# Optimization experiments

Hardware: AMD Instinct MI355X
Metric: run time of the kernel (lower is better)

## Reference

```python
import jax, jax.numpy as jnp
import numpy as np

NODE_NUMS = 128
IN_SIZE = 256
OUT_SIZE = 256
BATCH = 4096


def setup_inputs() -> dict:
    key = jax.random.key(0)
    k1, k2, k3, k4, k5 = jax.random.split(key, 5)
    # Xavier-uniform bounds
    limit_w = float(np.sqrt(6.0 / (IN_SIZE + OUT_SIZE)))
    limit_b = float(np.sqrt(6.0 / (NODE_NUMS + OUT_SIZE)))
    x = jax.random.normal(k1, (BATCH, IN_SIZE), dtype=jnp.float32)
    var_vector = jax.random.normal(k2, (BATCH, 16), dtype=jnp.float32)  # unused in forward
    W_1 = jax.random.uniform(k3, (NODE_NUMS, IN_SIZE, OUT_SIZE), dtype=jnp.float32,
                             minval=-limit_w, maxval=limit_w)
    b_1 = jax.random.uniform(k4, (NODE_NUMS, OUT_SIZE), dtype=jnp.float32,
                             minval=-limit_b, maxval=limit_b)
    node_ind = jax.random.randint(k5, (2, BATCH), 0, NODE_NUMS, dtype=jnp.int32)
    return {"x": x, "var_vector": var_vector, "W_1": W_1, "b_1": b_1, "node_ind": node_ind}


def reference(x, var_vector, W_1, b_1, node_ind):
    # idx selects a per-sample expert (node) weight matrix and bias.
    idx = node_ind[1]                       # [B]
    W = W_1[idx]                            # [B, in, out] gathered weights
    b = b_1[idx]                            # [B, out]
    # bmm(x[:,None,:], W).squeeze() + b  ==  einsum over the input dim
    return jnp.einsum('bi,bio->bo', x, W) + b
```

## Files before the change

### kernel.cpp

```cpp
#include <hip/hip_runtime.h>

#define BATCH 4096
#define INS   256
#define OUTS  256
#define NODES 128
#define NT    64
#define MCH   32

typedef short short8 __attribute__((ext_vector_type(8)));
typedef float f32x4  __attribute__((ext_vector_type(4)));

struct SMem {
    unsigned short list[BATCH];
    int cnt;
};

__device__ __forceinline__ unsigned short f2bf(float f) {
    unsigned int u = __builtin_bit_cast(unsigned int, f);
    u += 0x7fffu + ((u >> 16) & 1u);
    return (unsigned short)(u >> 16);
}

__device__ __forceinline__ short8 pack8(float4 a, float4 b) {
    short8 r;
    r[0] = (short)f2bf(a.x); r[1] = (short)f2bf(a.y);
    r[2] = (short)f2bf(a.z); r[3] = (short)f2bf(a.w);
    r[4] = (short)f2bf(b.x); r[5] = (short)f2bf(b.y);
    r[6] = (short)f2bf(b.z); r[7] = (short)f2bf(b.w);
    return r;
}

__global__ __launch_bounds__(256, 4) void moe_fwd(
    const float* __restrict__ x, const float* __restrict__ W1,
    const float* __restrict__ b1, const int* __restrict__ nid,
    float* __restrict__ out)
{
    __shared__ SMem sm;
    const int t   = threadIdx.x;
    const int bid = blockIdx.x;
    const int e  = (bid & 7) * 16 + ((bid >> 3) >> 2);
    const int c0 = ((bid >> 3) & 3) * NT;

    const int w  = t >> 6;
    const int l  = t & 63;
    const int g  = l >> 4;
    const int ln = l & 15;
    const int cc = c0 + w * 16 + ln;

    if (t == 0) sm.cnt = 0;
    __syncthreads();

    const float* __restrict__ wp = W1 + (size_t)e * (INS * OUTS) + cc;
    float wraw[64];
    #pragma unroll
    for (int ks = 0; ks < 8; ++ks) {
        #pragma unroll
        for (int j = 0; j < 8; ++j)
            wraw[ks * 8 + j] = wp[(size_t)(ks * 32 + g * 8 + j) * OUTS];
    }
    const float bval = b1[e * OUTS + cc];

    const int* __restrict__ idxp = nid + BATCH;
    #pragma unroll
    for (int it = 0; it < BATCH / 256; ++it) {
        int b = it * 256 + t;
        if (idxp[b] == e) {
            int p = atomicAdd(&sm.cnt, 1);
            sm.list[p] = (unsigned short)b;
        }
    }
    asm volatile("s_waitcnt lgkmcnt(0)" ::: "memory");
    __builtin_amdgcn_s_barrier();
    asm volatile("" ::: "memory");

    const int cnt = sm.cnt;
    if (cnt == 0) return;

    short8 wf[8];
    #pragma unroll
    for (int ks = 0; ks < 8; ++ks) {
        short8 v;
        #pragma unroll
        for (int j = 0; j < 8; ++j) v[j] = (short)f2bf(wraw[ks * 8 + j]);
        wf[ks] = v;
    }

    for (int m0 = 0; m0 < cnt; m0 += MCH) {
        int r0 = m0 + ln;
        int r1 = m0 + 16 + ln;
        int s0 = sm.list[r0 < cnt ? r0 : cnt - 1];
        int s1 = sm.list[r1 < cnt ? r1 : cnt - 1];
        const float* __restrict__ xp0 = x + (size_t)s0 * INS + g * 8;
        const float* __restrict__ xp1 = x + (size_t)s1 * INS + g * 8;

        f32x4 acc0 = {0.f, 0.f, 0.f, 0.f};
        f32x4 acc1 = {0.f, 0.f, 0.f, 0.f};
        #pragma unroll
        for (int ks = 0; ks < 8; ++ks) {
            float4 u0 = *reinterpret_cast<const float4*>(xp0 + ks * 32);
            float4 u1 = *reinterpret_cast<const float4*>(xp0 + ks * 32 + 4);
            float4 v0 = *reinterpret_cast<const float4*>(xp1 + ks * 32);
            float4 v1 = *reinterpret_cast<const float4*>(xp1 + ks * 32 + 4);
            short8 a0 = pack8(u0, u1);
            short8 a1 = pack8(v0, v1);
            acc0 = __builtin_amdgcn_mfma_f32_16x16x32_bf16(a0, wf[ks], acc0, 0, 0, 0);
            acc1 = __builtin_amdgcn_mfma_f32_16x16x32_bf16(a1, wf[ks], acc1, 0, 0, 0);
        }

        #pragma unroll
        for (int q = 0; q < 4; ++q) {
            int rr0 = m0 + g * 4 + q;
            if (rr0 < cnt)
                out[(size_t)sm.list[rr0] * OUTS + cc] = acc0[q] + bval;
            int rr1 = m0 + 16 + g * 4 + q;
            if (rr1 < cnt)
                out[(size_t)sm.list[rr1] * OUTS + cc] = acc1[q] + bval;
        }
    }
}

extern "C" void kernel_launch(void* const* d_in, const int* in_sizes, int n_in,
                              void* d_out, int out_size, void* d_ws, size_t ws_size,
                              hipStream_t stream) {
    const float* x   = (const float*)d_in[0];
    const float* W1  = (const float*)d_in[2];
    const float* b1  = (const float*)d_in[3];
    const int*   nid = (const int*)d_in[4];
    float* out = (float*)d_out;

    hipLaunchKernelGGL(moe_fwd, dim3(NODES * (OUTS / NT)), dim3(256), 0, stream,
                       x, W1, b1, nid, out);
}
```

Baseline: 25.41 us.

## Split batch range across two blocks per expert tile and shrink M chunk

Doubles the grid so each expert/column tile is handled by two blocks, each scanning half of the batch indices and processing only its matched rows. The M chunk is reduced from 32 to 16 rows, with a single accumulator per iteration. Weight bf16 conversion now happens at load time instead of being deferred until after the index scan. This aims to raise parallelism and occupancy, but the expert weight tile is now read twice from memory and the per-block scan overhead is duplicated.

```diff
diff --git a/kernel.cpp b/kernel.cpp
--- a/kernel.cpp
+++ b/kernel.cpp
@@ -5,13 +5,15 @@
 #define OUTS  256
 #define NODES 128
 #define NT    64
-#define MCH   32
+#define MCH   16
+#define MSPLIT 2
+#define MRANGE (BATCH / MSPLIT)
 
 typedef short short8 __attribute__((ext_vector_type(8)));
 typedef float f32x4  __attribute__((ext_vector_type(4)));
 
 struct SMem {
-    unsigned short list[BATCH];
+    unsigned short list[MRANGE];
     int cnt;
 };
 
@@ -38,8 +40,10 @@
     __shared__ SMem sm;
     const int t   = threadIdx.x;
     const int bid = blockIdx.x;
-    const int e  = (bid & 7) * 16 + ((bid >> 3) >> 2);
-    const int c0 = ((bid >> 3) & 3) * NT;
+    const int sub = bid >> 3;
+    const int e   = (bid & 7) * 16 + (sub >> 3);
+    const int c0  = ((sub >> 1) & 3) * NT;
+    const int mh  = sub & 1;
 
     const int w  = t >> 6;
     const int l  = t & 63;
@@ -51,22 +55,24 @@
     __syncthreads();
 
     const float* __restrict__ wp = W1 + (size_t)e * (INS * OUTS) + cc;
-    float wraw[64];
+    short8 wf[8];
     #pragma unroll
     for (int ks = 0; ks < 8; ++ks) {
+        short8 v;
         #pragma unroll
         for (int j = 0; j < 8; ++j)
-            wraw[ks * 8 + j] = wp[(size_t)(ks * 32 + g * 8 + j) * OUTS];
+            v[j] = (short)f2bf(wp[(size_t)(ks * 32 + g * 8 + j) * OUTS]);
+        wf[ks] = v;
     }
     const float bval = b1[e * OUTS + cc];
 
-    const int* __restrict__ idxp = nid + BATCH;
+    const int* __restrict__ idxp = nid + BATCH + mh * MRANGE;
     #pragma unroll
-    for (int it = 0; it < BATCH / 256; ++it) {
+    for (int it = 0; it < MRANGE / 256; ++it) {
         int b = it * 256 + t;
         if (idxp[b] == e) {
             int p = atomicAdd(&sm.cnt, 1);
-            sm.list[p] = (unsigned short)b;
+            sm.list[p] = (unsigned short)(mh * MRANGE + b);
         }
     }
     asm volatile("s_waitcnt lgkmcnt(0)" ::: "memory");
@@ -76,45 +82,25 @@
     const int cnt = sm.cnt;
     if (cnt == 0) return;
 
-    short8 wf[8];
-    #pragma unroll
-    for (int ks = 0; ks < 8; ++ks) {
-        short8 v;
-        #pragma unroll
-        for (int j = 0; j < 8; ++j) v[j] = (short)f2bf(wraw[ks * 8 + j]);
-        wf[ks] = v;
-    }
-
     for (int m0 = 0; m0 < cnt; m0 += MCH) {
         int r0 = m0 + ln;
-        int r1 = m0 + 16 + ln;
         int s0 = sm.list[r0 < cnt ? r0 : cnt - 1];
-        int s1 = sm.list[r1 < cnt ? r1 : cnt - 1];
         const float* __restrict__ xp0 = x + (size_t)s0 * INS + g * 8;
-        const float* __restrict__ xp1 = x + (size_t)s1 * INS + g * 8;
 
         f32x4 acc0 = {0.f, 0.f, 0.f, 0.f};
-        f32x4 acc1 = {0.f, 0.f, 0.f, 0.f};
         #pragma unroll
         for (int ks = 0; ks < 8; ++ks) {
             float4 u0 = *reinterpret_cast<const float4*>(xp0 + ks * 32);
             float4 u1 = *reinterpret_cast<const float4*>(xp0 + ks * 32 + 4);
-            float4 v0 = *reinterpret_cast<const float4*>(xp1 + ks * 32);
-            float4 v1 = *reinterpret_cast<const float4*>(xp1 + ks * 32 + 4);
             short8 a0 = pack8(u0, u1);
-            short8 a1 = pack8(v0, v1);
             acc0 = __builtin_amdgcn_mfma_f32_16x16x32_bf16(a0, wf[ks], acc0, 0, 0, 0);
-            acc1 = __builtin_amdgcn_mfma_f32_16x16x32_bf16(a1, wf[ks], acc1, 0, 0, 0);
         }
 
         #pragma unroll
         for (int q = 0; q < 4; ++q) {
-            int rr0 = m0 + g * 4 + q;
-            if (rr0 < cnt)
-                out[(size_t)sm.list[rr0] * OUTS + cc] = acc0[q] + bval;
-            int rr1 = m0 + 16 + g * 4 + q;
-            if (rr1 < cnt)
-                out[(size_t)sm.list[rr1] * OUTS + cc] = acc1[q] + bval;
+            int rr = m0 + g * 4 + q;
+            if (rr < cnt)
+                out[(size_t)sm.list[rr] * OUTS + cc] = acc0[q] + bval;
         }
     }
 }
@@ -128,6 +114,6 @@
     const int*   nid = (const int*)d_in[4];
     float* out = (float*)d_out;
 
-    hipLaunchKernelGGL(moe_fwd, dim3(NODES * (OUTS / NT)), dim3(256), 0, stream,
-                       x, W1, b1, nid, out);
+    hipLaunchKernelGGL(moe_fwd, dim3(NODES * (OUTS / NT) * MSPLIT), dim3(256),
+                       0, stream, x, W1, b1, nid, out);
 }
```

After: 24.38 us. 1.04x faster.
